# Kernel optimization log

Measured on AMD Instinct MI355X. Metric: run time of the kernel, lower is better.

Reference implementation:

```python
import jax, jax.numpy as jnp
import numpy as np

I, H, L = 128, 256, 64  # input_size, hidden_size, latent_dim
B, T = 64, 4096


def _lstm(x, h0, c0, Wih, Whh, bih, bhh):
    """x: [B,T,I]; returns (hs [B,T,H], hT [B,H]). PyTorch gate order i,f,g,o."""
    xg = jnp.einsum('bti,gi->btg', x, Wih) + bih  # precompute input projections

    def step(carry, xg_t):
        h, c = carry
        g = xg_t + h @ Whh.T + bhh
        i, f, gg, o = jnp.split(g, 4, axis=-1)
        c = jax.nn.sigmoid(f) * c + jax.nn.sigmoid(i) * jnp.tanh(gg)
        h = jax.nn.sigmoid(o) * jnp.tanh(c)
        return (h, c), h

    (hT, cT), hs = jax.lax.scan(step, (h0, c0), jnp.swapaxes(xg, 0, 1))
    return jnp.swapaxes(hs, 0, 1), hT


def setup_inputs() -> dict:
    key = jax.random.key(0)
    ks = jax.random.split(key, 20)
    s = 0.05
    d = {
        'padded_input': jax.random.normal(ks[0], (B, T, I), jnp.float32),
        'enc_Wih_f': jax.random.normal(ks[1], (4 * H, I), jnp.float32) * s,
        'enc_Whh_f': jax.random.normal(ks[2], (4 * H, H), jnp.float32) * s,
        'enc_bih_f': jax.random.normal(ks[3], (4 * H,), jnp.float32) * s,
        'enc_bhh_f': jax.random.normal(ks[4], (4 * H,), jnp.float32) * s,
        'enc_Wih_b': jax.random.normal(ks[5], (4 * H, I), jnp.float32) * s,
        'enc_Whh_b': jax.random.normal(ks[6], (4 * H, H), jnp.float32) * s,
        'enc_bih_b': jax.random.normal(ks[7], (4 * H,), jnp.float32) * s,
        'enc_bhh_b': jax.random.normal(ks[8], (4 * H,), jnp.float32) * s,
        'lat_W': jax.random.normal(ks[9], (L, 2 * H), jnp.float32) * s,
        'lat_b': jax.random.normal(ks[10], (L,), jnp.float32) * s,
        'l2h_W': jax.random.normal(ks[11], (H, L), jnp.float32) * s,
        'l2h_b': jax.random.normal(ks[12], (H,), jnp.float32) * s,
        'dec_Wih': jax.random.normal(ks[13], (4 * H, I), jnp.float32) * s,
        'dec_Whh': jax.random.normal(ks[14], (4 * H, H), jnp.float32) * s,
        'dec_bih': jax.random.normal(ks[15], (4 * H,), jnp.float32) * s,
        'dec_bhh': jax.random.normal(ks[16], (4 * H,), jnp.float32) * s,
        'out_W': jax.random.normal(ks[17], (I, H), jnp.float32) * s,
        'out_b': jax.random.normal(ks[18], (I,), jnp.float32) * s,
        'lengths': T,
    }
    return d


def reference(padded_input, enc_Wih_f, enc_Whh_f, enc_bih_f, enc_bhh_f,
              enc_Wih_b, enc_Whh_b, enc_bih_b, enc_bhh_b,
              lat_W, lat_b, l2h_W, l2h_b,
              dec_Wih, dec_Whh, dec_bih, dec_bhh, out_W, out_b, lengths):
    b = padded_input.shape[0]
    z = jnp.zeros((b, H), padded_input.dtype)
    # bidirectional encoder; only final hidden states are needed
    _, h_fwd = _lstm(padded_input, z, z, enc_Wih_f, enc_Whh_f, enc_bih_f, enc_bhh_f)
    _, h_bwd = _lstm(padded_input[:, ::-1], z, z, enc_Wih_b, enc_Whh_b, enc_bih_b, enc_bhh_b)
    h_n = jnp.concatenate([h_fwd, h_bwd], axis=1)  # [B, 2H]
    latent = h_n @ lat_W.T + lat_b                 # [B, L]
    hidden = latent @ l2h_W.T + l2h_b              # [B, H]
    # teacher forcing with ratio 1.0: decoder input at step t is padded_input[:, t-1]
    dec_in = padded_input[:, :-1]                  # [B, T-1, I]
    hs, _ = _lstm(dec_in, hidden, z, dec_Wih, dec_Whh, dec_bih, dec_bhh)
    decoded = jnp.einsum('bth,ih->bti', hs, out_W) + out_b  # [B, T-1, I]
    return decoded
```

## Files before the change

### kernel.cpp

```cpp
#include <hip/hip_runtime.h>
#include <stdint.h>

#define Ic 128
#define Hc 256

typedef uint32_t u32;
typedef unsigned long long u64;
using half2v = __attribute__((ext_vector_type(2))) _Float16;

__device__ __forceinline__ u32 pk_rne(float a, float b) {
    _Float16 lo = (_Float16)a, hi = (_Float16)b;
    return (u32)__builtin_bit_cast(uint16_t, lo) |
           ((u32)__builtin_bit_cast(uint16_t, hi) << 16);
}
__device__ __forceinline__ float dot2acc(u32 a, u32 b, float c) {
    return __builtin_amdgcn_fdot2(__builtin_bit_cast(half2v, a),
                                  __builtin_bit_cast(half2v, b), c, false);
}
__device__ __forceinline__ u32 rl(u32 v, int k) {
    return (u32)__builtin_amdgcn_readlane((int)v, k);
}
__device__ __forceinline__ float sigm(float x) {
    return __builtin_amdgcn_rcpf(1.f + __expf(-x));
}
__device__ __forceinline__ float tanh_f(float x) {
    float e = __expf(-2.f * __builtin_fabsf(x));
    float t = (1.f - e) * __builtin_amdgcn_rcpf(1.f + e);
    return __builtin_copysignf(t, x);
}
__device__ __forceinline__ u64 aload64(const u64* p) {
    return __hip_atomic_load(p, __ATOMIC_RELAXED, __HIP_MEMORY_SCOPE_AGENT);
}
__device__ __forceinline__ void astore64(u64* p, u64 v) {
    __hip_atomic_store(p, v, __ATOMIC_RELAXED, __HIP_MEMORY_SCOPE_AGENT);
}

__global__ __launch_bounds__(256, 1) void enc_kernel(
    const float* __restrict__ x,
    const float* __restrict__ WihF, const float* __restrict__ WhhF,
    const float* __restrict__ bihF, const float* __restrict__ bhhF,
    const float* __restrict__ WihB, const float* __restrict__ WhhB,
    const float* __restrict__ bihB, const float* __restrict__ bhhB,
    float* __restrict__ hF, float* __restrict__ hB,
    u64* __restrict__ xch,
    int T)
{
    const int t    = threadIdx.x;
    const int lane = t & 63;
    const int g    = blockIdx.x;
    const int half = (g >> 3) & 1;
    const int p    = ((g >> 4) << 3) | (g & 7);
    const int rev  = p >> 6;
    const int b    = p & 63;

    const int ug = t & 127;
    const int rA = (t >> 7) * Hc + half * 128 + ug;
    const int rB = ((t >> 7) + 2) * Hc + half * 128 + ug;

    const float* Wih = rev ? WihB : WihF;
    const float* Whh = rev ? WhhB : WhhF;
    const float* bih = rev ? bihB : bihF;
    const float* bhh = rev ? bhhB : bhhF;

    __shared__ u32   s_z[192];
    __shared__ float s_g[512];

    u32 whAo[64], whAp[64], wiA[64];
    u32 whBo[64], whBp[64], wiB[64];
    {
        const int ob = half * 64, pb2 = (half ^ 1) * 64;
        const float* wrA = Whh + (size_t)rA * Hc;
        const float* wrB = Whh + (size_t)rB * Hc;
#pragma unroll
        for (int j = 0; j < 64; j++) {
            whAo[j] = pk_rne(wrA[2*(ob+j)],  wrA[2*(ob+j)+1]);
            whBo[j] = pk_rne(wrB[2*(ob+j)],  wrB[2*(ob+j)+1]);
            whAp[j] = pk_rne(wrA[2*(pb2+j)], wrA[2*(pb2+j)+1]);
            whBp[j] = pk_rne(wrB[2*(pb2+j)], wrB[2*(pb2+j)+1]);
        }
        const float* irA = Wih + (size_t)rA * Ic;
        const float* irB = Wih + (size_t)rB * Ic;
#pragma unroll
        for (int j = 0; j < 64; j++) {
            wiA[j] = pk_rne(irA[2*j], irA[2*j+1]);
            wiB[j] = pk_rne(irB[2*j], irB[2*j+1]);
        }
    }
    const float biasA = bih[rA] + bhh[rA];
    const float biasB = bih[rB] + bhh[rB];

    u64* xch_self = xch + ((size_t)(p * 2 + half)) * 128;
    u64* xch_peer = xch + ((size_t)(p * 2 + (half ^ 1))) * 128;

    if (t < 64) s_z[t] = 0u;
    if (t >= 64 && t < 128) {
        int m = t - 64;
        int ts0 = rev ? (T - 1) : 0;
        const float* xp = x + ((size_t)b * T + ts0) * Ic + 2 * m;
        s_z[64 + m] = pk_rne(xp[0], xp[1]);
    }
    if (t >= 128 && t < 192) {
        int m = t - 128;
        int ts1 = rev ? (T - 2) : 1;
        const float* xp = x + ((size_t)b * T + ts1) * Ic + 2 * m;
        s_z[128 + m] = pk_rne(xp[0], xp[1]);
    }
    __syncthreads();

    float c0 = 0.f, c1 = 0.f;
    for (int s = 0; s < T; s++) {
        const u64* pslot = &xch_peer[(s & 1) * 64 + lane];
        u64 pv = 0;
        if (s > 0) pv = aload64(pslot);

        u32 vzx = s_z[64 + (s & 1) * 64 + lane];
        u32 vzo = s_z[lane];
        float aA0 = biasA, aA1 = 0.f, aA2 = 0.f, aA3 = 0.f;
        float aB0 = biasB, aB1 = 0.f, aB2 = 0.f, aB3 = 0.f;
#pragma unroll
        for (int k = 0; k < 64; k += 4) {
            u32 h0 = rl(vzx, k+0), h1 = rl(vzx, k+1), h2 = rl(vzx, k+2), h3 = rl(vzx, k+3);
            aA0 = dot2acc(h0, wiA[k+0], aA0); aB0 = dot2acc(h0, wiB[k+0], aB0);
            aA1 = dot2acc(h1, wiA[k+1], aA1); aB1 = dot2acc(h1, wiB[k+1], aB1);
            aA2 = dot2acc(h2, wiA[k+2], aA2); aB2 = dot2acc(h2, wiB[k+2], aB2);
            aA3 = dot2acc(h3, wiA[k+3], aA3); aB3 = dot2acc(h3, wiB[k+3], aB3);
        }
#pragma unroll
        for (int k = 0; k < 64; k += 4) {
            u32 h0 = rl(vzo, k+0), h1 = rl(vzo, k+1), h2 = rl(vzo, k+2), h3 = rl(vzo, k+3);
            aA0 = dot2acc(h0, whAo[k+0], aA0); aB0 = dot2acc(h0, whBo[k+0], aB0);
            aA1 = dot2acc(h1, whAo[k+1], aA1); aB1 = dot2acc(h1, whBo[k+1], aB1);
            aA2 = dot2acc(h2, whAo[k+2], aA2); aB2 = dot2acc(h2, whBo[k+2], aB2);
            aA3 = dot2acc(h3, whAo[k+3], aA3); aB3 = dot2acc(h3, whBo[k+3], aB3);
        }
        u32 vzp = 0u;
        if (s > 0) {
            while ((u32)(pv >> 32) < (u32)s) {
                __builtin_amdgcn_s_sleep(1);
                pv = aload64(pslot);
            }
            vzp = (u32)pv;
        }
#pragma unroll
        for (int k = 0; k < 64; k += 4) {
            u32 h0 = rl(vzp, k+0), h1 = rl(vzp, k+1), h2 = rl(vzp, k+2), h3 = rl(vzp, k+3);
            aA0 = dot2acc(h0, whAp[k+0], aA0); aB0 = dot2acc(h0, whBp[k+0], aB0);
            aA1 = dot2acc(h1, whAp[k+1], aA1); aB1 = dot2acc(h1, whBp[k+1], aB1);
            aA2 = dot2acc(h2, whAp[k+2], aA2); aB2 = dot2acc(h2, whBp[k+2], aB2);
            aA3 = dot2acc(h3, whAp[k+3], aA3); aB3 = dot2acc(h3, whBp[k+3], aB3);
        }
        s_g[t]       = (aA0 + aA1) + (aA2 + aA3);
        s_g[t + 256] = (aB0 + aB1) + (aB2 + aB3);
        __syncthreads();

        const int notlast = (s + 1 < T);
        if (t < 64) {
            float i0 = s_g[2*t],     i1 = s_g[2*t+1];
            float f0 = s_g[128+2*t], f1 = s_g[128+2*t+1];
            float g0 = s_g[256+2*t], g1 = s_g[256+2*t+1];
            float o0 = s_g[384+2*t], o1 = s_g[384+2*t+1];
            c0 = sigm(f0)*c0 + sigm(i0)*tanh_f(g0);
            c1 = sigm(f1)*c1 + sigm(i1)*tanh_f(g1);
            float h0 = sigm(o0)*tanh_f(c0);
            float h1 = sigm(o1)*tanh_f(c1);
            u32 hp = pk_rne(h0, h1);
            s_z[t] = hp;
            if (notlast) {
                astore64(&xch_self[((s+1) & 1) * 64 + t],
                         ((u64)(u32)(s + 1) << 32) | (u64)hp);
            } else {
                float* ho = (rev ? hB : hF) + (size_t)b * Hc + half * 128 + 2 * t;
                ho[0] = h0; ho[1] = h1;
            }
        } else if (t < 128) {
            int sn = s + 2;
            if (sn < T) {
                int m = t - 64;
                int ts = rev ? (T - 1 - sn) : sn;
                const float* xp = x + ((size_t)b * T + ts) * Ic + 2 * m;
                s_z[64 + (sn & 1) * 64 + m] = pk_rne(xp[0], xp[1]);
            }
        }
        __syncthreads();
    }
}

__global__ void lat_kernel(const float* __restrict__ hF, const float* __restrict__ hB,
                           const float* __restrict__ latW, const float* __restrict__ latb,
                           const float* __restrict__ l2hW, const float* __restrict__ l2hb,
                           float* __restrict__ hidden)
{
    int b = blockIdx.x, t = threadIdx.x;
    __shared__ float s_hn[512];
    __shared__ float s_lat[64];
    s_hn[t]       = hF[(size_t)b * Hc + t];
    s_hn[256 + t] = hB[(size_t)b * Hc + t];
    __syncthreads();
    if (t < 64) {
        float a = latb[t];
        const float* wp = latW + (size_t)t * 512;
        for (int k = 0; k < 512; k++) a += wp[k] * s_hn[k];
        s_lat[t] = a;
    }
    __syncthreads();
    float a = l2hb[t];
    const float* wp = l2hW + (size_t)t * 64;
#pragma unroll
    for (int k = 0; k < 64; k++) a += wp[k] * s_lat[k];
    hidden[(size_t)b * Hc + t] = a;
}

__global__ __launch_bounds__(256, 1) void dec_kernel(
    const float* __restrict__ x,
    const float* __restrict__ Wih, const float* __restrict__ Whh,
    const float* __restrict__ bih, const float* __restrict__ bhh,
    const float* __restrict__ outW, const float* __restrict__ outb,
    const float* __restrict__ hidden, float* __restrict__ out,
    u64* __restrict__ xch,
    int T)
{
    const int t    = threadIdx.x;
    const int lane = t & 63;
    const int g    = blockIdx.x;
    const int half = (g >> 3) & 1;
    const int b    = ((g >> 4) << 3) | (g & 7);
    const int Ts   = T - 1;

    const int ug = t & 127;
    const int rA = (t >> 7) * Hc + half * 128 + ug;
    const int rB = ((t >> 7) + 2) * Hc + half * 128 + ug;

    __shared__ u32   s_z[192];
    __shared__ float s_g[512];
    __shared__ float s_op[2][256];
    __shared__ u32   s_ow[32 * 256];

    u32 whAo[64], whAp[64], wiA[64];
    u32 whBo[64], whBp[64], wiB[64];
    {
        const int ob = half * 64, pb2 = (half ^ 1) * 64;
        const float* wrA = Whh + (size_t)rA * Hc;
        const float* wrB = Whh + (size_t)rB * Hc;
#pragma unroll
        for (int j = 0; j < 64; j++) {
            whAo[j] = pk_rne(wrA[2*(ob+j)],  wrA[2*(ob+j)+1]);
            whBo[j] = pk_rne(wrB[2*(ob+j)],  wrB[2*(ob+j)+1]);
            whAp[j] = pk_rne(wrA[2*(pb2+j)], wrA[2*(pb2+j)+1]);
            whBp[j] = pk_rne(wrB[2*(pb2+j)], wrB[2*(pb2+j)+1]);
        }
        const float* irA = Wih + (size_t)rA * Ic;
        const float* irB = Wih + (size_t)rB * Ic;
#pragma unroll
        for (int j = 0; j < 64; j++) {
            wiA[j] = pk_rne(irA[2*j], irA[2*j+1]);
            wiB[j] = pk_rne(irB[2*j], irB[2*j+1]);
        }
    }
    const float biasA = bih[rA] + bhh[rA];
    const float biasB = bih[rB] + bhh[rB];

    {
        const float* op = outW + (size_t)(half * 64 + (t & 63)) * Hc + (size_t)(t >> 6) * 64;
#pragma unroll
        for (int j = 0; j < 32; j++)
            s_ow[j * 256 + t] = pk_rne(op[2*j], op[2*j+1]);
    }
    const float outb_r = (t >= 128 && t < 192) ? outb[half * 64 + (t - 128)] : 0.f;

    u64* xch_self = xch + ((size_t)(b * 2 + half)) * 128;
    u64* xch_peer = xch + ((size_t)(b * 2 + (half ^ 1))) * 128;

    if (t < 64) {
        const float* hp = hidden + (size_t)b * Hc + half * 128 + 2 * t;
        s_z[t] = pk_rne(hp[0], hp[1]);
    }
    if (t >= 64 && t < 128) {
        int m = t - 64;
        const float* xp = x + ((size_t)b * T) * Ic + 2 * m;
        s_z[64 + m] = pk_rne(xp[0], xp[1]);
    }
    if (t >= 128 && t < 192) {
        int m = t - 128;
        const float* xp = x + ((size_t)b * T + 1) * Ic + 2 * m;
        s_z[128 + m] = pk_rne(xp[0], xp[1]);
    }
    u32 vzp_init;
    {
        const float* hp = hidden + (size_t)b * Hc + (half ^ 1) * 128 + 2 * lane;
        vzp_init = pk_rne(hp[0], hp[1]);
    }
    __syncthreads();

    float c0 = 0.f, c1 = 0.f;
    for (int s = 0; s < Ts; s++) {
        const u64* pslot = &xch_peer[(s & 1) * 64 + lane];
        u64 pv = 0;
        if (s > 0) pv = aload64(pslot);

        u32 vzx = s_z[64 + (s & 1) * 64 + lane];
        u32 vzo = s_z[lane];
        float aA0 = biasA, aA1 = 0.f, aA2 = 0.f, aA3 = 0.f;
        float aB0 = biasB, aB1 = 0.f, aB2 = 0.f, aB3 = 0.f;
#pragma unroll
        for (int k = 0; k < 64; k += 4) {
            u32 h0 = rl(vzx, k+0), h1 = rl(vzx, k+1), h2 = rl(vzx, k+2), h3 = rl(vzx, k+3);
            aA0 = dot2acc(h0, wiA[k+0], aA0); aB0 = dot2acc(h0, wiB[k+0], aB0);
            aA1 = dot2acc(h1, wiA[k+1], aA1); aB1 = dot2acc(h1, wiB[k+1], aB1);
            aA2 = dot2acc(h2, wiA[k+2], aA2); aB2 = dot2acc(h2, wiB[k+2], aB2);
            aA3 = dot2acc(h3, wiA[k+3], aA3); aB3 = dot2acc(h3, wiB[k+3], aB3);
        }
#pragma unroll
        for (int k = 0; k < 64; k += 4) {
            u32 h0 = rl(vzo, k+0), h1 = rl(vzo, k+1), h2 = rl(vzo, k+2), h3 = rl(vzo, k+3);
            aA0 = dot2acc(h0, whAo[k+0], aA0); aB0 = dot2acc(h0, whBo[k+0], aB0);
            aA1 = dot2acc(h1, whAo[k+1], aA1); aB1 = dot2acc(h1, whBo[k+1], aB1);
            aA2 = dot2acc(h2, whAo[k+2], aA2); aB2 = dot2acc(h2, whBo[k+2], aB2);
            aA3 = dot2acc(h3, whAo[k+3], aA3); aB3 = dot2acc(h3, whBo[k+3], aB3);
        }
        u32 vzp;
        if (s > 0) {
            while ((u32)(pv >> 32) < (u32)s) {
                __builtin_amdgcn_s_sleep(1);
                pv = aload64(pslot);
            }
            vzp = (u32)pv;
        } else vzp = vzp_init;
#pragma unroll
        for (int k = 0; k < 64; k += 4) {
            u32 h0 = rl(vzp, k+0), h1 = rl(vzp, k+1), h2 = rl(vzp, k+2), h3 = rl(vzp, k+3);
            aA0 = dot2acc(h0, whAp[k+0], aA0); aB0 = dot2acc(h0, whBp[k+0], aB0);
            aA1 = dot2acc(h1, whAp[k+1], aA1); aB1 = dot2acc(h1, whBp[k+1], aB1);
            aA2 = dot2acc(h2, whAp[k+2], aA2); aB2 = dot2acc(h2, whBp[k+2], aB2);
            aA3 = dot2acc(h3, whAp[k+3], aA3); aB3 = dot2acc(h3, whBp[k+3], aB3);
        }
        s_g[t]       = (aA0 + aA1) + (aA2 + aA3);
        s_g[t + 256] = (aB0 + aB1) + (aB2 + aB3);
        __syncthreads();

        if (t < 64) {
            float i0 = s_g[2*t],     i1 = s_g[2*t+1];
            float f0 = s_g[128+2*t], f1 = s_g[128+2*t+1];
            float g0 = s_g[256+2*t], g1 = s_g[256+2*t+1];
            float o0 = s_g[384+2*t], o1 = s_g[384+2*t+1];
            c0 = sigm(f0)*c0 + sigm(i0)*tanh_f(g0);
            c1 = sigm(f1)*c1 + sigm(i1)*tanh_f(g1);
            float h0 = sigm(o0)*tanh_f(c0);
            float h1 = sigm(o1)*tanh_f(c1);
            u32 hp = pk_rne(h0, h1);
            s_z[t] = hp;
            astore64(&xch_self[((s+1) & 1) * 64 + t],
                     ((u64)(u32)(s + 1) << 32) | (u64)hp);
        } else if (t < 128) {
            int sn = s + 2;
            if (sn < Ts) {
                int m = t - 64;
                const float* xp = x + ((size_t)b * T + sn) * Ic + 2 * m;
                s_z[64 + (sn & 1) * 64 + m] = pk_rne(xp[0], xp[1]);
            }
        } else if (t < 192 && s >= 2) {
            int rr = t - 128;
            const float* sp = s_op[(s - 1) & 1];
            float y = outb_r + ((sp[rr*4+0] + sp[rr*4+1]) + (sp[rr*4+2] + sp[rr*4+3]));
            out[((size_t)b * Ts + (s - 2)) * Ic + half * 64 + rr] = y;
        }
        if (s > 0) {
            const int ksl = t >> 6;
            const int kb  = (ksl & 1) * 32;
            u32 vplo = half ? vzp : vzo;
            u32 vphi = half ? vzo : vzp;
            float p0 = 0.f, p1 = 0.f;
#pragma unroll
            for (int j = 0; j < 32; j += 2) {
                u32 h0b = (ksl < 2) ? rl(vplo, kb + j)     : rl(vphi, kb + j);
                u32 h1b = (ksl < 2) ? rl(vplo, kb + j + 1) : rl(vphi, kb + j + 1);
                p0 = dot2acc(h0b, s_ow[(j)     * 256 + t], p0);
                p1 = dot2acc(h1b, s_ow[(j + 1) * 256 + t], p1);
            }
            s_op[s & 1][(t & 63) * 4 + ksl] = p0 + p1;
        }
        __syncthreads();
    }

    if (t >= 128 && t < 192) {
        int rr = t - 128;
        const float* sp = s_op[(Ts - 1) & 1];
        float y = outb_r + ((sp[rr*4+0] + sp[rr*4+1]) + (sp[rr*4+2] + sp[rr*4+3]));
        out[((size_t)b * Ts + (Ts - 2)) * Ic + half * 64 + rr] = y;
    }
    {
        u32 vzo2 = s_z[lane];
        const u64* pslot = &xch_peer[(Ts & 1) * 64 + lane];
        u64 pv = aload64(pslot);
        while ((u32)(pv >> 32) < (u32)Ts) {
            __builtin_amdgcn_s_sleep(1);
            pv = aload64(pslot);
        }
        u32 vzp2 = (u32)pv;
        const int ksl = t >> 6;
        const int kb  = (ksl & 1) * 32;
        u32 vplo = half ? vzp2 : vzo2;
        u32 vphi = half ? vzo2 : vzp2;
        float p0 = 0.f, p1 = 0.f;
#pragma unroll
        for (int j = 0; j < 32; j += 2) {
            u32 h0b = (ksl < 2) ? rl(vplo, kb + j)     : rl(vphi, kb + j);
            u32 h1b = (ksl < 2) ? rl(vplo, kb + j + 1) : rl(vphi, kb + j + 1);
            p0 = dot2acc(h0b, s_ow[(j)     * 256 + t], p0);
            p1 = dot2acc(h1b, s_ow[(j + 1) * 256 + t], p1);
        }
        s_op[Ts & 1][(t & 63) * 4 + ksl] = p0 + p1;
    }
    __syncthreads();
    if (t >= 128 && t < 192) {
        int rr = t - 128;
        const float* sp = s_op[Ts & 1];
        float y = outb_r + ((sp[rr*4+0] + sp[rr*4+1]) + (sp[rr*4+2] + sp[rr*4+3]));
        out[((size_t)b * Ts + (Ts - 1)) * Ic + half * 64 + rr] = y;
    }
}

extern "C" void kernel_launch(void* const* d_in, const int* in_sizes, int n_in,
                              void* d_out, int out_size, void* d_ws, size_t ws_size,
                              hipStream_t stream)
{
    const float* x    = (const float*)d_in[0];
    const float* WihF = (const float*)d_in[1];
    const float* WhhF = (const float*)d_in[2];
    const float* bihF = (const float*)d_in[3];
    const float* bhhF = (const float*)d_in[4];
    const float* WihB = (const float*)d_in[5];
    const float* WhhB = (const float*)d_in[6];
    const float* bihB = (const float*)d_in[7];
    const float* bhhB = (const float*)d_in[8];
    const float* latW = (const float*)d_in[9];
    const float* latb = (const float*)d_in[10];
    const float* l2hW = (const float*)d_in[11];
    const float* l2hb = (const float*)d_in[12];
    const float* dWih = (const float*)d_in[13];
    const float* dWhh = (const float*)d_in[14];
    const float* dbih = (const float*)d_in[15];
    const float* dbhh = (const float*)d_in[16];
    const float* outW = (const float*)d_in[17];
    const float* outb = (const float*)d_in[18];

    const int T = in_sizes[0] / (64 * Ic);

    float* ws  = (float*)d_ws;
    float* hFp = ws;
    float* hBp = ws + 16384;
    float* hid = ws + 32768;
    u64* encXch = (u64*)(ws + 49152);
    u64* decXch = encXch + 32768;

    hipMemsetAsync(encXch, 0, (32768 + 16384) * sizeof(u64), stream);

    enc_kernel<<<256, 256, 0, stream>>>(x, WihF, WhhF, bihF, bhhF,
                                        WihB, WhhB, bihB, bhhB,
                                        hFp, hBp, encXch, T);
    lat_kernel<<<64, 256, 0, stream>>>(hFp, hBp, latW, latb, l2hW, l2hb, hid);
    dec_kernel<<<128, 256, 0, stream>>>(x, dWih, dWhh, dbih, dbhh,
                                        outW, outb, hid, (float*)d_out,
                                        decXch, T);
}
```

Baseline: 30.37 ms.

## Remap gate rows per wave to compute LSTM cell in-register, one barrier per step

Each wavefront now owns 32 hidden units with the i/f/g/o gate rows for those units split across its two half-waves. The cell update is therefore done in registers with cross-lane shuffles, and the shared-memory gate buffer and one of the two block barriers per timestep are gone. The x input is prefetched into registers one step ahead instead of being staged through LDS. The h state is double-buffered in LDS and the barrier is a lightweight lgkmcnt wait plus s_barrier. The tradeoffs are extra shuffle instructions and redundant activation math across all 256 threads, in exchange for a shorter serial critical path per step.

```diff
diff --git a/kernel.cpp b/kernel.cpp
--- a/kernel.cpp
+++ b/kernel.cpp
@@ -33,6 +33,12 @@
 }
 __device__ __forceinline__ void astore64(u64* p, u64 v) {
     __hip_atomic_store(p, v, __ATOMIC_RELAXED, __HIP_MEMORY_SCOPE_AGENT);
+}
+__device__ __forceinline__ void block_sync_lds() {
+    asm volatile("s_waitcnt lgkmcnt(0)" ::: "memory");
+    __builtin_amdgcn_sched_barrier(0);
+    __builtin_amdgcn_s_barrier();
+    __builtin_amdgcn_sched_barrier(0);
 }
 
 __global__ __launch_bounds__(256, 1) void enc_kernel(
@@ -47,23 +53,25 @@
 {
     const int t    = threadIdx.x;
     const int lane = t & 63;
+    const int w    = t >> 6;
+    const int j    = lane & 31;
+    const int sel  = lane >> 5;
     const int g    = blockIdx.x;
     const int half = (g >> 3) & 1;
     const int p    = ((g >> 4) << 3) | (g & 7);
     const int rev  = p >> 6;
     const int b    = p & 63;
 
-    const int ug = t & 127;
-    const int rA = (t >> 7) * Hc + half * 128 + ug;
-    const int rB = ((t >> 7) + 2) * Hc + half * 128 + ug;
+    const int u  = half * 128 + w * 32 + j;
+    const int rA = sel * Hc + u;
+    const int rB = (sel + 2) * Hc + u;
 
     const float* Wih = rev ? WihB : WihF;
     const float* Whh = rev ? WhhB : WhhF;
     const float* bih = rev ? bihB : bihF;
     const float* bhh = rev ? bhhB : bhhF;
 
-    __shared__ u32   s_z[192];
-    __shared__ float s_g[512];
+    __shared__ u32 s_zh[2][64];
 
     u32 whAo[64], whAp[64], wiA[64];
     u32 whBo[64], whBp[64], wiB[64];
@@ -72,18 +80,18 @@
         const float* wrA = Whh + (size_t)rA * Hc;
         const float* wrB = Whh + (size_t)rB * Hc;
 #pragma unroll
-        for (int j = 0; j < 64; j++) {
-            whAo[j] = pk_rne(wrA[2*(ob+j)],  wrA[2*(ob+j)+1]);
-            whBo[j] = pk_rne(wrB[2*(ob+j)],  wrB[2*(ob+j)+1]);
-            whAp[j] = pk_rne(wrA[2*(pb2+j)], wrA[2*(pb2+j)+1]);
-            whBp[j] = pk_rne(wrB[2*(pb2+j)], wrB[2*(pb2+j)+1]);
+        for (int k = 0; k < 64; k++) {
+            whAo[k] = pk_rne(wrA[2*(ob+k)],  wrA[2*(ob+k)+1]);
+            whBo[k] = pk_rne(wrB[2*(ob+k)],  wrB[2*(ob+k)+1]);
+            whAp[k] = pk_rne(wrA[2*(pb2+k)], wrA[2*(pb2+k)+1]);
+            whBp[k] = pk_rne(wrB[2*(pb2+k)], wrB[2*(pb2+k)+1]);
         }
         const float* irA = Wih + (size_t)rA * Ic;
         const float* irB = Wih + (size_t)rB * Ic;
 #pragma unroll
-        for (int j = 0; j < 64; j++) {
-            wiA[j] = pk_rne(irA[2*j], irA[2*j+1]);
-            wiB[j] = pk_rne(irB[2*j], irB[2*j+1]);
+        for (int k = 0; k < 64; k++) {
+            wiA[k] = pk_rne(irA[2*k], irA[2*k+1]);
+            wiB[k] = pk_rne(irB[2*k], irB[2*k+1]);
         }
     }
     const float biasA = bih[rA] + bhh[rA];
@@ -92,29 +100,27 @@
     u64* xch_self = xch + ((size_t)(p * 2 + half)) * 128;
     u64* xch_peer = xch + ((size_t)(p * 2 + (half ^ 1))) * 128;
 
-    if (t < 64) s_z[t] = 0u;
-    if (t >= 64 && t < 128) {
-        int m = t - 64;
+    if (t < 64) { s_zh[0][t] = 0u; s_zh[1][t] = 0u; }
+    float2 xn;
+    {
         int ts0 = rev ? (T - 1) : 0;
-        const float* xp = x + ((size_t)b * T + ts0) * Ic + 2 * m;
-        s_z[64 + m] = pk_rne(xp[0], xp[1]);
-    }
-    if (t >= 128 && t < 192) {
-        int m = t - 128;
-        int ts1 = rev ? (T - 2) : 1;
-        const float* xp = x + ((size_t)b * T + ts1) * Ic + 2 * m;
-        s_z[128 + m] = pk_rne(xp[0], xp[1]);
+        xn = *(const float2*)(x + ((size_t)b * T + ts0) * Ic + 2 * lane);
     }
     __syncthreads();
 
-    float c0 = 0.f, c1 = 0.f;
+    float c = 0.f;
     for (int s = 0; s < T; s++) {
+        u32 vzx = pk_rne(xn.x, xn.y);
+        int sn = s + 1;
+        if (sn < T) {
+            int ts = rev ? (T - 1 - sn) : sn;
+            xn = *(const float2*)(x + ((size_t)b * T + ts) * Ic + 2 * lane);
+        }
         const u64* pslot = &xch_peer[(s & 1) * 64 + lane];
         u64 pv = 0;
         if (s > 0) pv = aload64(pslot);
 
-        u32 vzx = s_z[64 + (s & 1) * 64 + lane];
-        u32 vzo = s_z[lane];
+        u32 vzo = s_zh[s & 1][lane];
         float aA0 = biasA, aA1 = 0.f, aA2 = 0.f, aA3 = 0.f;
         float aB0 = biasB, aB1 = 0.f, aB2 = 0.f, aB3 = 0.f;
 #pragma unroll
@@ -149,39 +155,28 @@
             aA2 = dot2acc(h2, whAp[k+2], aA2); aB2 = dot2acc(h2, whBp[k+2], aB2);
             aA3 = dot2acc(h3, whAp[k+3], aA3); aB3 = dot2acc(h3, whBp[k+3], aB3);
         }
-        s_g[t]       = (aA0 + aA1) + (aA2 + aA3);
-        s_g[t + 256] = (aB0 + aB1) + (aB2 + aB3);
-        __syncthreads();
-
+        float aAs = (aA0 + aA1) + (aA2 + aA3);
+        float aBs = (aB0 + aB1) + (aB2 + aB3);
+
+        float f_ = __shfl(aAs, 32 + j);
+        float o_ = __shfl(aBs, 32 + j);
+        c = sigm(f_) * c + sigm(aAs) * tanh_f(aBs);
+        float h = sigm(o_) * tanh_f(c);
+        float he = __shfl(h, 2 * (lane & 15));
+        float ho = __shfl(h, 2 * (lane & 15) + 1);
+        u32 hp = pk_rne(he, ho);
         const int notlast = (s + 1 < T);
-        if (t < 64) {
-            float i0 = s_g[2*t],     i1 = s_g[2*t+1];
-            float f0 = s_g[128+2*t], f1 = s_g[128+2*t+1];
-            float g0 = s_g[256+2*t], g1 = s_g[256+2*t+1];
-            float o0 = s_g[384+2*t], o1 = s_g[384+2*t+1];
-            c0 = sigm(f0)*c0 + sigm(i0)*tanh_f(g0);
-            c1 = sigm(f1)*c1 + sigm(i1)*tanh_f(g1);
-            float h0 = sigm(o0)*tanh_f(c0);
-            float h1 = sigm(o1)*tanh_f(c1);
-            u32 hp = pk_rne(h0, h1);
-            s_z[t] = hp;
-            if (notlast) {
-                astore64(&xch_self[((s+1) & 1) * 64 + t],
+        if (lane < 16) {
+            int q = w * 16 + lane;
+            s_zh[(s + 1) & 1][q] = hp;
+            if (notlast)
+                astore64(&xch_self[((s + 1) & 1) * 64 + q],
                          ((u64)(u32)(s + 1) << 32) | (u64)hp);
-            } else {
-                float* ho = (rev ? hB : hF) + (size_t)b * Hc + half * 128 + 2 * t;
-                ho[0] = h0; ho[1] = h1;
-            }
-        } else if (t < 128) {
-            int sn = s + 2;
-            if (sn < T) {
-                int m = t - 64;
-                int ts = rev ? (T - 1 - sn) : sn;
-                const float* xp = x + ((size_t)b * T + ts) * Ic + 2 * m;
-                s_z[64 + (sn & 1) * 64 + m] = pk_rne(xp[0], xp[1]);
-            }
-        }
-        __syncthreads();
+        }
+        if (!notlast && lane < 32) {
+            (rev ? hB : hF)[(size_t)b * Hc + u] = h;
+        }
+        block_sync_lds();
     }
 }
 
@@ -221,17 +216,19 @@
 {
     const int t    = threadIdx.x;
     const int lane = t & 63;
+    const int w    = t >> 6;
+    const int j    = lane & 31;
+    const int sel  = lane >> 5;
     const int g    = blockIdx.x;
     const int half = (g >> 3) & 1;
     const int b    = ((g >> 4) << 3) | (g & 7);
     const int Ts   = T - 1;
 
-    const int ug = t & 127;
-    const int rA = (t >> 7) * Hc + half * 128 + ug;
-    const int rB = ((t >> 7) + 2) * Hc + half * 128 + ug;
-
-    __shared__ u32   s_z[192];
-    __shared__ float s_g[512];
+    const int u  = half * 128 + w * 32 + j;
+    const int rA = sel * Hc + u;
+    const int rB = (sel + 2) * Hc + u;
+
+    __shared__ u32   s_zh[2][64];
     __shared__ float s_op[2][256];
     __shared__ u32   s_ow[32 * 256];
 
@@ -242,18 +239,18 @@
         const float* wrA = Whh + (size_t)rA * Hc;
         const float* wrB = Whh + (size_t)rB * Hc;
 #pragma unroll
-        for (int j = 0; j < 64; j++) {
-            whAo[j] = pk_rne(wrA[2*(ob+j)],  wrA[2*(ob+j)+1]);
-            whBo[j] = pk_rne(wrB[2*(ob+j)],  wrB[2*(ob+j)+1]);
-            whAp[j] = pk_rne(wrA[2*(pb2+j)], wrA[2*(pb2+j)+1]);
-            whBp[j] = pk_rne(wrB[2*(pb2+j)], wrB[2*(pb2+j)+1]);
+        for (int k = 0; k < 64; k++) {
+            whAo[k] = pk_rne(wrA[2*(ob+k)],  wrA[2*(ob+k)+1]);
+            whBo[k] = pk_rne(wrB[2*(ob+k)],  wrB[2*(ob+k)+1]);
+            whAp[k] = pk_rne(wrA[2*(pb2+k)], wrA[2*(pb2+k)+1]);
+            whBp[k] = pk_rne(wrB[2*(pb2+k)], wrB[2*(pb2+k)+1]);
         }
         const float* irA = Wih + (size_t)rA * Ic;
         const float* irB = Wih + (size_t)rB * Ic;
 #pragma unroll
-        for (int j = 0; j < 64; j++) {
-            wiA[j] = pk_rne(irA[2*j], irA[2*j+1]);
-            wiB[j] = pk_rne(irB[2*j], irB[2*j+1]);
+        for (int k = 0; k < 64; k++) {
+            wiA[k] = pk_rne(irA[2*k], irA[2*k+1]);
+            wiB[k] = pk_rne(irB[2*k], irB[2*k+1]);
         }
     }
     const float biasA = bih[rA] + bhh[rA];
@@ -262,43 +259,38 @@
     {
         const float* op = outW + (size_t)(half * 64 + (t & 63)) * Hc + (size_t)(t >> 6) * 64;
 #pragma unroll
-        for (int j = 0; j < 32; j++)
-            s_ow[j * 256 + t] = pk_rne(op[2*j], op[2*j+1]);
-    }
-    const float outb_r = (t >= 128 && t < 192) ? outb[half * 64 + (t - 128)] : 0.f;
+        for (int k = 0; k < 32; k++)
+            s_ow[k * 256 + t] = pk_rne(op[2*k], op[2*k+1]);
+    }
+    const float outb_r = (lane >= 32 && lane < 48) ? outb[half * 64 + w * 16 + (lane - 32)] : 0.f;
 
     u64* xch_self = xch + ((size_t)(b * 2 + half)) * 128;
     u64* xch_peer = xch + ((size_t)(b * 2 + (half ^ 1))) * 128;
 
     if (t < 64) {
         const float* hp = hidden + (size_t)b * Hc + half * 128 + 2 * t;
-        s_z[t] = pk_rne(hp[0], hp[1]);
-    }
-    if (t >= 64 && t < 128) {
-        int m = t - 64;
-        const float* xp = x + ((size_t)b * T) * Ic + 2 * m;
-        s_z[64 + m] = pk_rne(xp[0], xp[1]);
-    }
-    if (t >= 128 && t < 192) {
-        int m = t - 128;
-        const float* xp = x + ((size_t)b * T + 1) * Ic + 2 * m;
-        s_z[128 + m] = pk_rne(xp[0], xp[1]);
+        u32 v = pk_rne(hp[0], hp[1]);
+        s_zh[0][t] = v; s_zh[1][t] = v;
     }
     u32 vzp_init;
     {
         const float* hp = hidden + (size_t)b * Hc + (half ^ 1) * 128 + 2 * lane;
         vzp_init = pk_rne(hp[0], hp[1]);
     }
+    float2 xn = *(const float2*)(x + ((size_t)b * T) * Ic + 2 * lane);
     __syncthreads();
 
-    float c0 = 0.f, c1 = 0.f;
+    float c = 0.f;
     for (int s = 0; s < Ts; s++) {
+        u32 vzx = pk_rne(xn.x, xn.y);
+        int sn = s + 1;
+        if (sn < Ts)
+            xn = *(const float2*)(x + ((size_t)b * T + sn) * Ic + 2 * lane);
         const u64* pslot = &xch_peer[(s & 1) * 64 + lane];
         u64 pv = 0;
         if (s > 0) pv = aload64(pslot);
 
-        u32 vzx = s_z[64 + (s & 1) * 64 + lane];
-        u32 vzo = s_z[lane];
+        u32 vzo = s_zh[s & 1][lane];
         float aA0 = biasA, aA1 = 0.f, aA2 = 0.f, aA3 = 0.f;
         float aB0 = biasB, aB1 = 0.f, aB2 = 0.f, aB3 = 0.f;
 #pragma unroll
@@ -333,36 +325,23 @@
             aA2 = dot2acc(h2, whAp[k+2], aA2); aB2 = dot2acc(h2, whBp[k+2], aB2);
             aA3 = dot2acc(h3, whAp[k+3], aA3); aB3 = dot2acc(h3, whBp[k+3], aB3);
         }
-        s_g[t]       = (aA0 + aA1) + (aA2 + aA3);
-        s_g[t + 256] = (aB0 + aB1) + (aB2 + aB3);
-        __syncthreads();
-
-        if (t < 64) {
-            float i0 = s_g[2*t],     i1 = s_g[2*t+1];
-            float f0 = s_g[128+2*t], f1 = s_g[128+2*t+1];
-            float g0 = s_g[256+2*t], g1 = s_g[256+2*t+1];
-            float o0 = s_g[384+2*t], o1 = s_g[384+2*t+1];
-            c0 = sigm(f0)*c0 + sigm(i0)*tanh_f(g0);
-            c1 = sigm(f1)*c1 + sigm(i1)*tanh_f(g1);
-            float h0 = sigm(o0)*tanh_f(c0);
-            float h1 = sigm(o1)*tanh_f(c1);
-            u32 hp = pk_rne(h0, h1);
-            s_z[t] = hp;
-            astore64(&xch_self[((s+1) & 1) * 64 + t],
+        float aAs = (aA0 + aA1) + (aA2 + aA3);
+        float aBs = (aB0 + aB1) + (aB2 + aB3);
+
+        float f_ = __shfl(aAs, 32 + j);
+        float o_ = __shfl(aBs, 32 + j);
+        c = sigm(f_) * c + sigm(aAs) * tanh_f(aBs);
+        float h = sigm(o_) * tanh_f(c);
+        float he = __shfl(h, 2 * (lane & 15));
+        float ho = __shfl(h, 2 * (lane & 15) + 1);
+        u32 hp = pk_rne(he, ho);
+        if (lane < 16) {
+            int q = w * 16 + lane;
+            s_zh[(s + 1) & 1][q] = hp;
+            astore64(&xch_self[((s + 1) & 1) * 64 + q],
                      ((u64)(u32)(s + 1) << 32) | (u64)hp);
-        } else if (t < 128) {
-            int sn = s + 2;
-            if (sn < Ts) {
-                int m = t - 64;
-                const float* xp = x + ((size_t)b * T + sn) * Ic + 2 * m;
-                s_z[64 + (sn & 1) * 64 + m] = pk_rne(xp[0], xp[1]);
-            }
-        } else if (t < 192 && s >= 2) {
-            int rr = t - 128;
-            const float* sp = s_op[(s - 1) & 1];
-            float y = outb_r + ((sp[rr*4+0] + sp[rr*4+1]) + (sp[rr*4+2] + sp[rr*4+3]));
-            out[((size_t)b * Ts + (s - 2)) * Ic + half * 64 + rr] = y;
-        }
+        }
+
         if (s > 0) {
             const int ksl = t >> 6;
             const int kb  = (ksl & 1) * 32;
@@ -370,25 +349,31 @@
             u32 vphi = half ? vzo : vzp;
             float p0 = 0.f, p1 = 0.f;
 #pragma unroll
-            for (int j = 0; j < 32; j += 2) {
-                u32 h0b = (ksl < 2) ? rl(vplo, kb + j)     : rl(vphi, kb + j);
-                u32 h1b = (ksl < 2) ? rl(vplo, kb + j + 1) : rl(vphi, kb + j + 1);
-                p0 = dot2acc(h0b, s_ow[(j)     * 256 + t], p0);
-                p1 = dot2acc(h1b, s_ow[(j + 1) * 256 + t], p1);
+            for (int k = 0; k < 32; k += 2) {
+                u32 h0b = (ksl < 2) ? rl(vplo, kb + k)     : rl(vphi, kb + k);
+                u32 h1b = (ksl < 2) ? rl(vplo, kb + k + 1) : rl(vphi, kb + k + 1);
+                p0 = dot2acc(h0b, s_ow[(k)     * 256 + t], p0);
+                p1 = dot2acc(h1b, s_ow[(k + 1) * 256 + t], p1);
             }
             s_op[s & 1][(t & 63) * 4 + ksl] = p0 + p1;
         }
-        __syncthreads();
-    }
-
-    if (t >= 128 && t < 192) {
-        int rr = t - 128;
+        if (s >= 2 && lane >= 32 && lane < 48) {
+            int r = w * 16 + (lane - 32);
+            const float* sp = s_op[(s - 1) & 1];
+            float y = outb_r + ((sp[r*4+0] + sp[r*4+1]) + (sp[r*4+2] + sp[r*4+3]));
+            out[((size_t)b * Ts + (s - 2)) * Ic + half * 64 + r] = y;
+        }
+        block_sync_lds();
+    }
+
+    if (lane >= 32 && lane < 48) {
+        int r = w * 16 + (lane - 32);
         const float* sp = s_op[(Ts - 1) & 1];
-        float y = outb_r + ((sp[rr*4+0] + sp[rr*4+1]) + (sp[rr*4+2] + sp[rr*4+3]));
-        out[((size_t)b * Ts + (Ts - 2)) * Ic + half * 64 + rr] = y;
-    }
-    {
-        u32 vzo2 = s_z[lane];
+        float y = outb_r + ((sp[r*4+0] + sp[r*4+1]) + (sp[r*4+2] + sp[r*4+3]));
+        out[((size_t)b * Ts + (Ts - 2)) * Ic + half * 64 + r] = y;
+    }
+    {
+        u32 vzo2 = s_zh[Ts & 1][lane];
         const u64* pslot = &xch_peer[(Ts & 1) * 64 + lane];
         u64 pv = aload64(pslot);
         while ((u32)(pv >> 32) < (u32)Ts) {
@@ -402,20 +387,20 @@
         u32 vphi = half ? vzo2 : vzp2;
         float p0 = 0.f, p1 = 0.f;
 #pragma unroll
-        for (int j = 0; j < 32; j += 2) {
-            u32 h0b = (ksl < 2) ? rl(vplo, kb + j)     : rl(vphi, kb + j);
-            u32 h1b = (ksl < 2) ? rl(vplo, kb + j + 1) : rl(vphi, kb + j + 1);
-            p0 = dot2acc(h0b, s_ow[(j)     * 256 + t], p0);
-            p1 = dot2acc(h1b, s_ow[(j + 1) * 256 + t], p1);
+        for (int k = 0; k < 32; k += 2) {
+            u32 h0b = (ksl < 2) ? rl(vplo, kb + k)     : rl(vphi, kb + k);
+            u32 h1b = (ksl < 2) ? rl(vplo, kb + k + 1) : rl(vphi, kb + k + 1);
+            p0 = dot2acc(h0b, s_ow[(k)     * 256 + t], p0);
+            p1 = dot2acc(h1b, s_ow[(k + 1) * 256 + t], p1);
         }
         s_op[Ts & 1][(t & 63) * 4 + ksl] = p0 + p1;
     }
-    __syncthreads();
-    if (t >= 128 && t < 192) {
-        int rr = t - 128;
+    block_sync_lds();
+    if (lane >= 32 && lane < 48) {
+        int r = w * 16 + (lane - 32);
         const float* sp = s_op[Ts & 1];
-        float y = outb_r + ((sp[rr*4+0] + sp[rr*4+1]) + (sp[rr*4+2] + sp[rr*4+3]));
-        out[((size_t)b * Ts + (Ts - 1)) * Ic + half * 64 + rr] = y;
+        float y = outb_r + ((sp[r*4+0] + sp[r*4+1]) + (sp[r*4+2] + sp[r*4+3]));
+        out[((size_t)b * Ts + (Ts - 1)) * Ic + half * 64 + r] = y;
     }
 }
 
```

New measurement: 30.19 ms. No clear change (-0.6%).
